# Optimization experiments

Hardware: AMD Instinct MI355X
Metric: run time of the kernel (lower is better)

Reference implementation:

```python
import jax, jax.numpy as jnp
import numpy as np

BATCH, IN_DIM, GRID, HID, DEPTH = 2048, 128, 128, 256, 7
BN_EPS = 1e-5


def setup_inputs() -> dict:
    key = jax.random.key(0)
    ks = jax.random.split(key, 10)
    x = jax.random.uniform(ks[0], (BATCH, IN_DIM), dtype=jnp.float32)
    grids = jax.random.uniform(ks[1], (DEPTH, IN_DIM, GRID), dtype=jnp.float32)  # torch.rand init
    fs = jax.random.normal(ks[2], (DEPTH, IN_DIM, GRID, HID), dtype=jnp.float32)
    depth_scores = jnp.ones((DEPTH,), dtype=jnp.float32)
    mlp_W = jax.random.normal(ks[3], (3, HID, HID), dtype=jnp.float32) * (1.0 / np.sqrt(HID))
    mlp_b = jnp.zeros((3, HID), dtype=jnp.float32)
    bn_gamma = jnp.ones((3, HID), dtype=jnp.float32)
    bn_beta = jnp.zeros((3, HID), dtype=jnp.float32)
    W_out = jax.random.normal(ks[4], (HID, 1), dtype=jnp.float32) * (1.0 / np.sqrt(HID))
    b_out = jnp.zeros((1,), dtype=jnp.float32)
    return {"x": x, "grids": grids, "fs": fs, "depth_scores": depth_scores,
            "mlp_W": mlp_W, "mlp_b": mlp_b, "bn_gamma": bn_gamma,
            "bn_beta": bn_beta, "W_out": W_out, "b_out": b_out}


def reference(x, grids, fs, depth_scores, mlp_W, mlp_b, bn_gamma, bn_beta, W_out, b_out):
    # per-feature min-max normalization over the batch dim
    xmin = x.min(axis=0, keepdims=True)
    xmax = x.max(axis=0, keepdims=True)
    z = (x - xmin) / (xmax - xmin + 1e-6)  # [B, I]

    outputs = []
    for i in range(DEPTH):
        Bmat = jax.nn.relu(z[:, :, None] - grids[i][None, :, :])  # [B, I, G]
        # (B.unsqueeze(-1) * fs[i]).sum(2).sum(1) == einsum big,igh->bh
        H = jnp.einsum('big,igh->bh', Bmat, fs[i])  # [B, H]
        if i > 0:  # residual accumulation
            H = H + outputs[-1]
        outputs.append(H)
    stacked = jnp.stack(outputs, axis=0)  # [D, B, H]
    w = jax.nn.softmax(depth_scores)  # depth attention
    h = jnp.einsum('d,dbh->bh', w, stacked)

    # MLP head (BatchNorm uses batch stats = training-mode behaviour; Dropout off)
    for j in range(3):
        h = h @ mlp_W[j] + mlp_b[j]
        mean = h.mean(axis=0)
        var = h.var(axis=0)  # biased, matching torch BN normalization
        h = (h - mean) * jax.lax.rsqrt(var + BN_EPS) * bn_gamma[j] + bn_beta[j]
        h = jax.nn.gelu(h, approximate=False)  # torch nn.GELU is exact erf GELU
    return h @ W_out + b_out
```

## Files before the change

kernel.cpp:

```cpp
#include <hip/hip_runtime.h>
#include <hip/hip_bf16.h>

#define BATCH 2048
#define IN_DIM 128
#define GRIDN 128
#define HID 256
#define DEPTH 7

typedef unsigned int u32;
typedef __attribute__((ext_vector_type(8))) short short8;
typedef __attribute__((ext_vector_type(4))) float floatx4;

#define OFF_FST   ((size_t)0)
#define SZ_FST    ((size_t)7*128*256*128*2)
#define OFF_ZT    (OFF_FST + SZ_FST)
#define SZ_ZT     ((size_t)BATCH*IN_DIM*4)
#define OFF_HPRE  (OFF_ZT + SZ_ZT)
#define SZ_HPRE   ((size_t)BATCH*HID*4)
#define OFF_STATS (OFF_HPRE + SZ_HPRE)
#define SZ_STATS  ((size_t)3*2*HID*4)
#define OFF_KEYS  (OFF_STATS + SZ_STATS)
#define SZ_KEYS   ((size_t)256*4)
#define OFF_CW    (OFF_KEYS + SZ_KEYS)
#define SZ_CW     ((size_t)32)
#define OFF_Y1    (OFF_CW + SZ_CW)
#define SZ_Y      ((size_t)BATCH*HID*4)
#define OFF_Y2    (OFF_Y1 + SZ_Y)
#define OFF_Y3    (OFF_Y2 + SZ_Y)

__device__ __forceinline__ void gload_lds16(const void* g, void* l) {
  __builtin_amdgcn_global_load_lds(
      (const __attribute__((address_space(1))) u32*)g,
      (__attribute__((address_space(3))) u32*)l, 16, 0, 0);
}

__device__ __forceinline__ u32 pack2_bf16(float lo, float hi) {
  __hip_bfloat162 b2;
  b2.x = __float2bfloat16(lo);
  b2.y = __float2bfloat16(hi);
  return *reinterpret_cast<u32*>(&b2);
}

__device__ __forceinline__ u32 pk_trunc(float a, float b) {
  return __builtin_amdgcn_perm(__float_as_uint(b), __float_as_uint(a), 0x07060302u);
}

__device__ __forceinline__ float gelu_exact(float x) {
  return 0.5f * x * (1.0f + erff(x * 0.70710678118654752f));
}

__global__ void prep1_kernel(const float* __restrict__ x, u32* __restrict__ keys,
                             const float* __restrict__ depth_scores,
                             float* __restrict__ cw) {
  int t = threadIdx.x;
  int base = blockIdx.x * 256 + t;
  float mn = 1e30f, mx = -1e30f;
#pragma unroll
  for (int j = 0; j < 16; ++j) {
    float v = x[base + j * 16384];
    mn = fminf(mn, v); mx = fmaxf(mx, v);
  }
  __shared__ float smn[256], smx[256];
  smn[t] = mn; smx[t] = mx;
  __syncthreads();
  if (t < 128) {
    mn = fminf(smn[t], smn[t + 128]);
    mx = fmaxf(smx[t], smx[t + 128]);
    int i = base & 127;
    atomicMax(&keys[i], 0x7FFFFFFFu - __float_as_uint(mn));
    atomicMax(&keys[128 + i], __float_as_uint(mx));
  }
  if (blockIdx.x == 0 && t == 0) {
    float m = -1e30f;
    for (int d0 = 0; d0 < DEPTH; ++d0) m = fmaxf(m, depth_scores[d0]);
    float e[DEPTH]; float sum = 0.f;
    for (int d0 = 0; d0 < DEPTH; ++d0) { e[d0] = expf(depth_scores[d0] - m); sum += e[d0]; }
    float cacc = 0.f; float cs[DEPTH];
    for (int d0 = DEPTH - 1; d0 >= 0; --d0) { cacc += e[d0] / sum; cs[d0] = cacc; }
    for (int d0 = 0; d0 < DEPTH; ++d0) cw[d0] = cs[d0];
  }
}

__global__ void prep2_kernel(const float* __restrict__ x, const u32* __restrict__ keys,
                             float* __restrict__ z_t) {
  __shared__ float lds[128 * 65];
  int t = threadIdx.x;
  int b0 = blockIdx.x * 64;
#pragma unroll
  for (int q = 0; q < 32; ++q) {
    int idx = q * 256 + t;
    int b = idx >> 7, i = idx & 127;
    lds[i * 65 + b] = x[(size_t)(b0 + b) * IN_DIM + i];
  }
  __syncthreads();
#pragma unroll
  for (int q = 0; q < 32; ++q) {
    int idx = q * 256 + t;
    int ii = idx >> 6, bb = idx & 63;
    float mnv = __uint_as_float(0x7FFFFFFFu - keys[ii]);
    float mxv = __uint_as_float(keys[128 + ii]);
    float v = (lds[ii * 65 + bb] - mnv) * (1.0f / (mxv - mnv + 1e-6f));
    z_t[(size_t)ii * BATCH + b0 + bb] = v;
  }
}

__global__ void convert_kernel(const float* __restrict__ fs,
                               const float* __restrict__ cw,
                               __hip_bfloat16* __restrict__ fs2) {
  __shared__ u32 lds[256 * 33];
  int slab = blockIdx.x;
  int t = threadIdx.x;
  float cd = cw[slab >> 7];
  const float* src = fs + (size_t)slab * (GRIDN * HID);
  char* dstb = (char*)fs2 + (size_t)slab * 65536;

  for (int gh = 0; gh < 2; ++gh) {
    const float* s0 = src + (size_t)gh * 64 * HID + t;
#pragma unroll
    for (int g2 = 0; g2 < 32; ++g2) {
      float va = s0[(size_t)(2 * g2) * HID];
      float vb = s0[(size_t)(2 * g2 + 1) * HID];
      lds[t * 33 + g2] = pack2_bf16(cd * va, cd * vb);
    }
    __syncthreads();
#pragma unroll
    for (int it2 = 0; it2 < 8; ++it2) {
      int task = t + it2 * 256;
      int c = task >> 9;
      int q = task & 511;
      int nhalf = c >> 1, ksl = c & 1;
      int tt = q >> 6, l4 = (q >> 4) & 3, l15 = q & 15;
      int h = nhalf * 128 + tt * 16 + l15;
      int m = ksl * 4 + l4;
      u32 a0 = lds[h * 33 + m * 4 + 0];
      u32 a1 = lds[h * 33 + m * 4 + 1];
      u32 a2 = lds[h * 33 + m * 4 + 2];
      u32 a3 = lds[h * 33 + m * 4 + 3];
      size_t off = (size_t)nhalf * 32768 + (size_t)(gh * 2 + ksl) * 8192 +
                   (size_t)tt * 1024 + l4 * 256 + l15 * 16;
      *(uint4*)(dstb + off) = make_uint4(a0, a1, a2, a3);
    }
    __syncthreads();
  }
}

__launch_bounds__(256, 2)
__global__ void gemm_kernel(const float* __restrict__ z_t,
                            const float* __restrict__ grids,
                            const __hip_bfloat16* __restrict__ fs2,
                            float* __restrict__ h_pre) {
  __shared__ __align__(16) char lds[65536];

  int bx = blockIdx.x;
  int xcd = bx & 7;
  int t6 = bx >> 3;
  int cg = t6 >> 4;
  int jb = t6 & 15;
  int chunk = xcd + 8 * cg;
  int slab0 = chunk * 28;

  int tid = threadIdx.x;
  int w = tid >> 6, l = tid & 63;
  int l15 = l & 15, l4 = l >> 4;
  int wm = w >> 1;
  int wn = w & 1;
  int mbase = jb * 128 + wm * 64;
  int nbase = wn * 128;
  char* mylds = lds + w * 16384;

  floatx4 acc[4][8];
#pragma unroll
  for (int a = 0; a < 4; ++a)
#pragma unroll
    for (int b = 0; b < 8; ++b) acc[a][b] = (floatx4)0.f;

  const char* fsb = (const char*)fs2 + (size_t)slab0 * 65536 + (size_t)wn * 32768 +
                    (size_t)l * 16;

  auto stage = [&](int step, int p) {
    const char* srcb = fsb + (size_t)(step >> 2) * 65536 + (size_t)(step & 3) * 8192;
    char* dst = mylds + p * 8192;
#pragma unroll
    for (int j = 0; j < 8; ++j)
      gload_lds16(srcb + j * 1024, dst + j * 1024);
  };

  float zv[2][4];
  float4 g0[2], g1[2];
  auto loadzg = [&](int step, int p) {
    int slab = slab0 + (step >> 2);
    int iz = slab & 127;
    const float* zp = z_t + (size_t)iz * BATCH + mbase + l15;
    zv[p][0] = zp[0]; zv[p][1] = zp[16]; zv[p][2] = zp[32]; zv[p][3] = zp[48];
    const float* gp = grids + (size_t)slab * GRIDN + (step & 3) * 32 + l4 * 8;
    g0[p] = *(const float4*)gp;
    g1[p] = *(const float4*)(gp + 4);
  };

  loadzg(0, 0);
  stage(0, 0);

#pragma unroll 2
  for (int step = 0; step < 112; ++step) {
    int p = step & 1;
    __builtin_amdgcn_s_waitcnt(0x0F70);
    __asm__ volatile("" ::: "memory");

    short8 bf[8];
#pragma unroll
    for (int tt = 0; tt < 8; ++tt)
      bf[tt] = *(const short8*)(mylds + p * 8192 + tt * 1024 + l * 16);
    __asm__ volatile("" ::: "memory");

    if (step + 1 < 112) stage(step + 1, p ^ 1);

    short8 af[4];
#pragma unroll
    for (int u = 0; u < 4; ++u) {
      float zu = zv[p][u];
      union { uint4 q; short8 s8; } pk;
      pk.q.x = pk_trunc(fmaxf(zu - g0[p].x, 0.f), fmaxf(zu - g0[p].y, 0.f));
      pk.q.y = pk_trunc(fmaxf(zu - g0[p].z, 0.f), fmaxf(zu - g0[p].w, 0.f));
      pk.q.z = pk_trunc(fmaxf(zu - g1[p].x, 0.f), fmaxf(zu - g1[p].y, 0.f));
      pk.q.w = pk_trunc(fmaxf(zu - g1[p].z, 0.f), fmaxf(zu - g1[p].w, 0.f));
      af[u] = pk.s8;
    }

    if (step + 1 < 112) loadzg(step + 1, p ^ 1);

#pragma unroll
    for (int u = 0; u < 4; ++u)
#pragma unroll
      for (int tt = 0; tt < 8; ++tt)
        acc[u][tt] = __builtin_amdgcn_mfma_f32_16x16x32_bf16(af[u], bf[tt], acc[u][tt], 0, 0, 0);
  }

  int row0 = mbase + l4 * 4;
  int col0 = nbase + l15;
#pragma unroll
  for (int u = 0; u < 4; ++u) {
#pragma unroll
    for (int tt = 0; tt < 8; ++tt) {
      int col = col0 + tt * 16;
#pragma unroll
      for (int r = 0; r < 4; ++r) {
        int row = row0 + u * 16 + r;
        atomicAdd(&h_pre[(size_t)row * HID + col], acc[u][tt][r]);
      }
    }
  }
}

template <int FIRST>
__global__ void mlp_kernel(const float* __restrict__ Xin,
                           const float* __restrict__ statsIn,
                           const float* __restrict__ gamma,
                           const float* __restrict__ beta,
                           const float* __restrict__ W,
                           const float* __restrict__ bias,
                           float* __restrict__ Yout,
                           float* __restrict__ statsOut) {
  __shared__ float Xs[4][HID];
  int br = blockIdx.x, c = threadIdx.x;
  float mean = 0.f, rstd = 1.f, gm = 1.f, bt = 0.f;
  if (!FIRST) {
    float s1 = statsIn[c], s2 = statsIn[HID + c];
    mean = s1 * (1.0f / BATCH);
    float var = s2 * (1.0f / BATCH) - mean * mean;
    rstd = rsqrtf(var + 1e-5f);
    gm = gamma[c]; bt = beta[c];
  }
#pragma unroll
  for (int r = 0; r < 4; ++r) {
    float v = Xin[(size_t)(br * 4 + r) * HID + c];
    if (!FIRST) v = gelu_exact((v - mean) * rstd * gm + bt);
    Xs[r][c] = v;
  }
  __syncthreads();
  float acc[4] = {0, 0, 0, 0};
#pragma unroll 8
  for (int k = 0; k < HID; ++k) {
    float wv = W[(size_t)k * HID + c];
#pragma unroll
    for (int r = 0; r < 4; ++r) acc[r] += Xs[r][k] * wv;
  }
  float bb = bias[c];
  float s1 = 0.f, s2 = 0.f;
#pragma unroll
  for (int r = 0; r < 4; ++r) {
    float y = acc[r] + bb;
    Yout[(size_t)(br * 4 + r) * HID + c] = y;
    s1 += y; s2 += y * y;
  }
  atomicAdd(&statsOut[c], s1);
  atomicAdd(&statsOut[HID + c], s2);
}

__global__ void final_kernel(const float* __restrict__ Y3,
                             const float* __restrict__ statsIn,
                             const float* __restrict__ gamma,
                             const float* __restrict__ beta,
                             const float* __restrict__ W_out,
                             const float* __restrict__ b_out,
                             float* __restrict__ out) {
  int w = threadIdx.x >> 6, l = threadIdx.x & 63;
  int b = blockIdx.x * 4 + w;
  float4 y = *(const float4*)(Y3 + (size_t)b * HID + l * 4);
  float4 wv = *(const float4*)(W_out + l * 4);
  float r4[4] = {y.x, y.y, y.z, y.w};
  float w4[4] = {wv.x, wv.y, wv.z, wv.w};
  float s = 0.f;
  int c0 = l * 4;
#pragma unroll
  for (int q = 0; q < 4; ++q) {
    int c = c0 + q;
    float s1 = statsIn[c], s2 = statsIn[HID + c];
    float mean = s1 * (1.0f / BATCH);
    float var = s2 * (1.0f / BATCH) - mean * mean;
    float rstd = rsqrtf(var + 1e-5f);
    float v = gelu_exact((r4[q] - mean) * rstd * gamma[c] + beta[c]);
    s += v * w4[q];
  }
#pragma unroll
  for (int off = 32; off > 0; off >>= 1) s += __shfl_down(s, off);
  if (l == 0) out[b] = s + b_out[0];
}

extern "C" void kernel_launch(void* const* d_in, const int* in_sizes, int n_in,
                              void* d_out, int out_size, void* d_ws, size_t ws_size,
                              hipStream_t stream) {
  const float* x      = (const float*)d_in[0];
  const float* grids  = (const float*)d_in[1];
  const float* fs     = (const float*)d_in[2];
  const float* dscore = (const float*)d_in[3];
  const float* mlp_W  = (const float*)d_in[4];
  const float* mlp_b  = (const float*)d_in[5];
  const float* bn_g   = (const float*)d_in[6];
  const float* bn_b   = (const float*)d_in[7];
  const float* W_out  = (const float*)d_in[8];
  const float* b_out  = (const float*)d_in[9];
  float* out = (float*)d_out;

  char* ws = (char*)d_ws;
  __hip_bfloat16* fs2 = (__hip_bfloat16*)(ws + OFF_FST);
  float* z_t   = (float*)(ws + OFF_ZT);
  float* h_pre = (float*)(ws + OFF_HPRE);
  float* stats = (float*)(ws + OFF_STATS);
  u32*   keys  = (u32*)(ws + OFF_KEYS);
  float* cw    = (float*)(ws + OFF_CW);
  float* Y1    = (float*)(ws + OFF_Y1);
  float* Y2    = (float*)(ws + OFF_Y2);
  float* Y3    = (float*)(ws + OFF_Y3);

  hipMemsetAsync(h_pre, 0, SZ_HPRE + SZ_STATS + SZ_KEYS, stream);

  prep1_kernel<<<64, 256, 0, stream>>>(x, keys, dscore, cw);
  prep2_kernel<<<32, 256, 0, stream>>>(x, keys, z_t);
  convert_kernel<<<DEPTH * IN_DIM, 256, 0, stream>>>(fs, cw, fs2);
  gemm_kernel<<<512, 256, 0, stream>>>(z_t, grids, fs2, h_pre);

  mlp_kernel<1><<<512, 256, 0, stream>>>(h_pre, nullptr, nullptr, nullptr,
                                         mlp_W, mlp_b, Y1, stats);
  mlp_kernel<0><<<512, 256, 0, stream>>>(Y1, stats, bn_g, bn_b,
                                         mlp_W + 65536, mlp_b + 256, Y2, stats + 512);
  mlp_kernel<0><<<512, 256, 0, stream>>>(Y2, stats + 512, bn_g + 256, bn_b + 256,
                                         mlp_W + 2 * 65536, mlp_b + 2 * 256, Y3, stats + 1024);
  final_kernel<<<512, 256, 0, stream>>>(Y3, stats + 1024, bn_g + 512, bn_b + 512,
                                        W_out, b_out, out);
}
```

Before: 453.3 us.

## Deepen GEMM pipeline to four half-step LDS buffers with partial vmcnt waits

```diff
diff --git a/kernel.cpp b/kernel.cpp
--- a/kernel.cpp
+++ b/kernel.cpp
@@ -144,6 +144,12 @@
   }
 }
 
+#define FENCE __asm__ volatile("" ::: "memory")
+#define WAITV(c) do { __builtin_amdgcn_s_waitcnt(c); FENCE; } while (0)
+#define VM14 0x0F7E
+#define VM4  0x0F74
+#define VM0  0x0F70
+
 __launch_bounds__(256, 2)
 __global__ void gemm_kernel(const float* __restrict__ z_t,
                             const float* __restrict__ grids,
@@ -177,63 +183,103 @@
   const char* fsb = (const char*)fs2 + (size_t)slab0 * 65536 + (size_t)wn * 32768 +
                     (size_t)l * 16;
 
-  auto stage = [&](int step, int p) {
-    const char* srcb = fsb + (size_t)(step >> 2) * 65536 + (size_t)(step & 3) * 8192;
-    char* dst = mylds + p * 8192;
-#pragma unroll
-    for (int j = 0; j < 8; ++j)
+  auto stage4 = [&](int u) {
+    const char* srcb = fsb + (size_t)(u >> 3) * 65536 + (size_t)((u >> 1) & 3) * 8192 +
+                       (size_t)(u & 1) * 4096;
+    char* dst = mylds + (u & 3) * 4096;
+#pragma unroll
+    for (int j = 0; j < 4; ++j)
       gload_lds16(srcb + j * 1024, dst + j * 1024);
   };
 
-  float zv[2][4];
-  float4 g0[2], g1[2];
-  auto loadzg = [&](int step, int p) {
-    int slab = slab0 + (step >> 2);
+  float4 zA, zB;
+  float4 g0A, g1A, g0B, g1B;
+  auto zgload = [&](int s, float4& zv, float4& G0, float4& G1) {
+    int slab = slab0 + (s >> 2);
     int iz = slab & 127;
     const float* zp = z_t + (size_t)iz * BATCH + mbase + l15;
-    zv[p][0] = zp[0]; zv[p][1] = zp[16]; zv[p][2] = zp[32]; zv[p][3] = zp[48];
-    const float* gp = grids + (size_t)slab * GRIDN + (step & 3) * 32 + l4 * 8;
-    g0[p] = *(const float4*)gp;
-    g1[p] = *(const float4*)(gp + 4);
+    zv.x = zp[0]; zv.y = zp[16]; zv.z = zp[32]; zv.w = zp[48];
+    const float* gp = grids + (size_t)slab * GRIDN + (s & 3) * 32 + l4 * 8;
+    G0 = *(const float4*)gp;
+    G1 = *(const float4*)(gp + 4);
   };
 
-  loadzg(0, 0);
-  stage(0, 0);
-
-#pragma unroll 2
-  for (int step = 0; step < 112; ++step) {
-    int p = step & 1;
-    __builtin_amdgcn_s_waitcnt(0x0F70);
-    __asm__ volatile("" ::: "memory");
-
-    short8 bf[8];
-#pragma unroll
-    for (int tt = 0; tt < 8; ++tt)
-      bf[tt] = *(const short8*)(mylds + p * 8192 + tt * 1024 + l * 16);
-    __asm__ volatile("" ::: "memory");
-
-    if (step + 1 < 112) stage(step + 1, p ^ 1);
-
-    short8 af[4];
+  short8 af[4];
+  short8 bf[4];
+  auto rdfrag = [&](const int bufIdx) {
+    const char* bp = mylds + bufIdx * 4096 + l * 16;
+    bf[0] = *(const short8*)(bp);
+    bf[1] = *(const short8*)(bp + 1024);
+    bf[2] = *(const short8*)(bp + 2048);
+    bf[3] = *(const short8*)(bp + 3072);
+  };
+  auto afgen = [&](const float4 zv, const float4 G0, const float4 G1) {
 #pragma unroll
     for (int u = 0; u < 4; ++u) {
-      float zu = zv[p][u];
+      float zu = (u == 0) ? zv.x : (u == 1) ? zv.y : (u == 2) ? zv.z : zv.w;
       union { uint4 q; short8 s8; } pk;
-      pk.q.x = pk_trunc(fmaxf(zu - g0[p].x, 0.f), fmaxf(zu - g0[p].y, 0.f));
-      pk.q.y = pk_trunc(fmaxf(zu - g0[p].z, 0.f), fmaxf(zu - g0[p].w, 0.f));
-      pk.q.z = pk_trunc(fmaxf(zu - g1[p].x, 0.f), fmaxf(zu - g1[p].y, 0.f));
-      pk.q.w = pk_trunc(fmaxf(zu - g1[p].z, 0.f), fmaxf(zu - g1[p].w, 0.f));
+      pk.q.x = pk_trunc(fmaxf(zu - G0.x, 0.f), fmaxf(zu - G0.y, 0.f));
+      pk.q.y = pk_trunc(fmaxf(zu - G0.z, 0.f), fmaxf(zu - G0.w, 0.f));
+      pk.q.z = pk_trunc(fmaxf(zu - G1.x, 0.f), fmaxf(zu - G1.y, 0.f));
+      pk.q.w = pk_trunc(fmaxf(zu - G1.z, 0.f), fmaxf(zu - G1.w, 0.f));
       af[u] = pk.s8;
     }
-
-    if (step + 1 < 112) loadzg(step + 1, p ^ 1);
-
-#pragma unroll
-    for (int u = 0; u < 4; ++u)
-#pragma unroll
-      for (int tt = 0; tt < 8; ++tt)
-        acc[u][tt] = __builtin_amdgcn_mfma_f32_16x16x32_bf16(af[u], bf[tt], acc[u][tt], 0, 0, 0);
-  }
+  };
+  auto mfma16 = [&](const int ttBase) {
+    __builtin_amdgcn_s_setprio(1);
+#pragma unroll
+    for (int u = 0; u < 4; ++u) {
+      acc[u][ttBase + 0] = __builtin_amdgcn_mfma_f32_16x16x32_bf16(af[u], bf[0], acc[u][ttBase + 0], 0, 0, 0);
+      acc[u][ttBase + 1] = __builtin_amdgcn_mfma_f32_16x16x32_bf16(af[u], bf[1], acc[u][ttBase + 1], 0, 0, 0);
+      acc[u][ttBase + 2] = __builtin_amdgcn_mfma_f32_16x16x32_bf16(af[u], bf[2], acc[u][ttBase + 2], 0, 0, 0);
+      acc[u][ttBase + 3] = __builtin_amdgcn_mfma_f32_16x16x32_bf16(af[u], bf[3], acc[u][ttBase + 3], 0, 0, 0);
+    }
+    __builtin_amdgcn_s_setprio(0);
+  };
+
+  zgload(0, zA, g0A, g1A); FENCE;
+  stage4(0); stage4(1); stage4(2); FENCE;
+  zgload(1, zB, g0B, g1B); FENCE;
+
+#pragma unroll 1
+  for (int s = 0; s < 110; s += 2) {
+    WAITV(VM14);
+    stage4(2 * s + 3); FENCE;
+    rdfrag(0);
+    afgen(zA, g0A, g1A);
+    mfma16(0);
+    WAITV(VM14);
+    stage4(2 * s + 4); FENCE;
+    zgload(s + 2, zA, g0A, g1A); FENCE;
+    rdfrag(1);
+    mfma16(4);
+    WAITV(VM14);
+    stage4(2 * s + 5); FENCE;
+    rdfrag(2);
+    afgen(zB, g0B, g1B);
+    mfma16(0);
+    WAITV(VM14);
+    stage4(2 * s + 6); FENCE;
+    zgload(s + 3, zB, g0B, g1B); FENCE;
+    rdfrag(3);
+    mfma16(4);
+  }
+
+  WAITV(VM14);
+  stage4(223); FENCE;
+  rdfrag(0);
+  afgen(zA, g0A, g1A);
+  mfma16(0);
+  WAITV(VM14);
+  rdfrag(1);
+  mfma16(4);
+  WAITV(VM4);
+  rdfrag(2);
+  afgen(zB, g0B, g1B);
+  mfma16(0);
+  WAITV(VM0);
+  rdfrag(3);
+  mfma16(4);
 
   int row0 = mbase + l4 * 4;
   int col0 = nbase + l15;
```

Measured after the change: 439.5 us. 1.03x faster.
